# Performance work log

Measured on AMD Instinct MI355X. Metric: run time of the kernel, lower is better.

Reference implementation:

```python
import jax, jax.numpy as jnp
import numpy as np

EPS = 1e-7  # keras backend epsilon
ROUTINGS = 3

def squash(s, axis=-1):
    # v = ||s||^2/(1+||s||^2) * s/||s||
    sq = jnp.sum(jnp.square(s), axis=axis, keepdims=True)
    scale = sq / (1.0 + sq) / jnp.sqrt(sq + EPS)
    return scale * s

def setup_inputs() -> dict:
    key = jax.random.key(0)
    k1, k2 = jax.random.split(key)
    B, in_num, in_dim = 64, 2048, 16
    num_caps, dim_caps = 64, 32
    inputs = jax.random.normal(k1, (B, in_num, in_dim), dtype=jnp.float32)
    # glorot_uniform limit = sqrt(6/(fan_in+fan_out)) with fan_in=in_dim, fan_out=dim_caps
    limit = np.sqrt(6.0 / (in_dim + dim_caps)).astype(np.float32)
    W = jax.random.uniform(k2, (num_caps, in_num, dim_caps, in_dim),
                           dtype=jnp.float32, minval=-limit, maxval=limit)
    return {"inputs": inputs, "W": W}

def reference(inputs, W):
    # inputs: [b, i, l]; W: [j, i, k, l]
    # inputs_hat[b, j, i, k] = W[j, i, k, :] @ inputs[b, i, :]
    u_hat = jnp.einsum('jikl,bil->bjik', W, inputs)
    B, J, I, K = u_hat.shape
    b = jnp.zeros((B, J, I), dtype=u_hat.dtype)  # routing logits
    v = None
    for r in range(ROUTINGS):
        c = jax.nn.softmax(b, axis=1)                      # softmax over output capsules j
        s = jnp.einsum('bji,bjik->bjk', c, u_hat)          # weighted sum over input capsules
        v = squash(s)                                      # [b, j, k]
        if r < ROUTINGS - 1:
            b = b + jnp.einsum('bjk,bjik->bji', v, u_hat)  # agreement update
    return v  # [B, num_capsule, dim_capsule]
```

## Files before the change

kernel.cpp:

```cpp
#include <hip/hip_runtime.h>


#define B_ 64
#define I_ 2048
#define L_ 16
#define J_ 64
#define K_ 32
#define N_ 2048

typedef _Float16 half8_t __attribute__((ext_vector_type(8)));
typedef float f32x16 __attribute__((ext_vector_type(16)));
typedef float float4_t __attribute__((ext_vector_type(4)));

__device__ __forceinline__ f32x16 fzero16() {
    f32x16 z;
#pragma unroll
    for (int r = 0; r < 16; ++r) z[r] = 0.f;
    return z;
}

__global__ __launch_bounds__(256) void cast_x_kernel(const float* __restrict__ X,
                                                     _Float16* __restrict__ Xh) {
    unsigned tid = blockIdx.x * 256u + threadIdx.x;
    unsigned b = tid & 63u;
    unsigned i = tid >> 6;
    const float4_t* src = (const float4_t*)(X + (size_t)(b * I_ + i) * L_);
    float4_t f0 = src[0], f1 = src[1], f2 = src[2], f3 = src[3];
    half8_t h0, h1;
#pragma unroll
    for (int e = 0; e < 4; ++e) {
        h0[e] = (_Float16)f0[e];
        h0[4 + e] = (_Float16)f1[e];
        h1[e] = (_Float16)f2[e];
        h1[4 + e] = (_Float16)f3[e];
    }
    _Float16* dst = Xh + (size_t)(i * B_ + b) * L_;
    *(half8_t*)dst = h0;
    *(half8_t*)(dst + 8) = h1;
}

__global__ __launch_bounds__(512) void s0_cast_kernel(const float* __restrict__ Wf,
                                                      _Float16* __restrict__ Wh_out,
                                                      const _Float16* __restrict__ Xh,
                                                      _Float16* __restrict__ parts,
                                                      int SCH, int ICH) {
    const int tid = threadIdx.x;
    const int w = tid >> 6;
    const int l = tid & 63;
    const int h2 = l >> 5;
    const int kb = l & 31;
    const int chunk = blockIdx.x >> 3;
    const int jq = blockIdx.x & 7;
    const int j = jq * 8 + w;

    float s0[16], s1[16];
#pragma unroll
    for (int r = 0; r < 16; ++r) { s0[r] = 0.f; s1[r] = 0.f; }

    const int i0 = chunk * ICH;
    for (int ii = 0; ii < ICH; ++ii) {
        const int i = i0 + ii;
        const _Float16* xb = Xh + (size_t)i * (B_ * L_);
        half8_t xf0 = *(const half8_t*)(xb + kb * L_ + 8 * h2);
        half8_t xf1 = *(const half8_t*)(xb + (32 + kb) * L_ + 8 * h2);
        const float4_t* wsrc =
            (const float4_t*)(Wf + ((size_t)(j * I_ + i) * K_ + kb) * L_ + 8 * h2);
        float4_t a0 = wsrc[0], a1 = wsrc[1];
        half8_t af;
#pragma unroll
        for (int e = 0; e < 4; ++e) {
            af[e] = (_Float16)a0[e];
            af[4 + e] = (_Float16)a1[e];
        }
        *(half8_t*)(Wh_out + ((size_t)(i * J_ + j) * K_ + kb) * L_ + 8 * h2) = af;
        f32x16 acc0 = __builtin_amdgcn_mfma_f32_32x32x16_f16(af, xf0, fzero16(), 0, 0, 0);
        f32x16 acc1 = __builtin_amdgcn_mfma_f32_32x32x16_f16(af, xf1, fzero16(), 0, 0, 0);
#pragma unroll
        for (int r = 0; r < 16; ++r) {
            s0[r] += acc0[r];
            s1[r] += acc1[r];
        }
    }
#pragma unroll
    for (int r = 0; r < 16; ++r) {
        const int k = (r & 3) + 8 * (r >> 2) + 4 * h2;
        _Float16* p = parts + (((size_t)chunk * J_ + j) * K_ + k) * B_;
        p[kb] = (_Float16)s0[r];
        p[32 + kb] = (_Float16)s1[r];
    }
}

__global__ __launch_bounds__(512, 6) void zcalc_kernel(const _Float16* __restrict__ Wh,
                                                       const _Float16* __restrict__ Xh,
                                                       const _Float16* __restrict__ wvz,
                                                       _Float16* __restrict__ ebuf,
                                                       int SCH, int ICH) {
    const int tid = threadIdx.x;
    const int w = tid >> 6;
    const int l = tid & 63;
    const int h2 = l >> 5;
    const int kb = l & 31;
    const int chunk = blockIdx.x >> 3;
    const int jq = blockIdx.x & 7;
    const int j = jq * 8 + w;

    const _Float16* wp = wvz + ((size_t)(j * 2 + h2) * B_ + kb) * 16;
    const half8_t wv00 = *(const half8_t*)wp;
    const half8_t wv01 = *(const half8_t*)(wp + 8);
    const half8_t wv10 = *(const half8_t*)(wp + 512);
    const half8_t wv11 = *(const half8_t*)(wp + 520);

    const int i0 = chunk * ICH;
    for (int ii = 0; ii < ICH; ++ii) {
        const int i = i0 + ii;
        const _Float16* xb = Xh + (size_t)i * (B_ * L_);
        half8_t xf0 = *(const half8_t*)(xb + kb * L_ + 8 * h2);
        half8_t xf1 = *(const half8_t*)(xb + (32 + kb) * L_ + 8 * h2);
        half8_t af = *(const half8_t*)(Wh + ((size_t)(i * J_ + j) * K_ + kb) * L_ + 8 * h2);
        f32x16 acc0 = __builtin_amdgcn_mfma_f32_32x32x16_f16(af, xf0, fzero16(), 0, 0, 0);
        f32x16 acc1 = __builtin_amdgcn_mfma_f32_32x32x16_f16(af, xf1, fzero16(), 0, 0, 0);
        float z0a = 0.f, z0b = 0.f, z0c = 0.f, z0d = 0.f;
        float z1a = 0.f, z1b = 0.f, z1c = 0.f, z1d = 0.f;
#pragma unroll
        for (int r = 0; r < 4; ++r) {
            z0a += acc0[r]      * (float)wv00[r];
            z0b += acc0[r + 4]  * (float)wv00[r + 4];
            z0c += acc0[r + 8]  * (float)wv01[r];
            z0d += acc0[r + 12] * (float)wv01[r + 4];
            z1a += acc1[r]      * (float)wv10[r];
            z1b += acc1[r + 4]  * (float)wv10[r + 4];
            z1c += acc1[r + 8]  * (float)wv11[r];
            z1d += acc1[r + 12] * (float)wv11[r + 4];
        }
        float z0 = (z0a + z0b) + (z0c + z0d);
        float z1 = (z1a + z1b) + (z1c + z1d);
        z0 += __shfl_xor(z0, 32, 64);
        z1 += __shfl_xor(z1, 32, 64);
        const float zf = fminf((l < 32) ? z0 : z1, 11.0f);
        ebuf[((size_t)j * I_ + i) * B_ + l] = (_Float16)__expf(zf);
    }
}

__global__ __launch_bounds__(256, 8) void dsum_kernel(const _Float16* __restrict__ ebuf,
                                                      float* __restrict__ rD) {
    const int w = threadIdx.x >> 6;
    const int l = threadIdx.x & 63;
    const int i = blockIdx.x * 4 + w;
    float p0 = 0.f, p1 = 0.f, p2 = 0.f, p3 = 0.f;
#pragma unroll
    for (int jq = 0; jq < 16; ++jq) {
        p0 += (float)ebuf[((size_t)(jq * 4 + 0) * I_ + i) * B_ + l];
        p1 += (float)ebuf[((size_t)(jq * 4 + 1) * I_ + i) * B_ + l];
        p2 += (float)ebuf[((size_t)(jq * 4 + 2) * I_ + i) * B_ + l];
        p3 += (float)ebuf[((size_t)(jq * 4 + 3) * I_ + i) * B_ + l];
    }
    rD[i * B_ + l] = 1.0f / ((p0 + p1) + (p2 + p3));
}

__global__ __launch_bounds__(512) void s_kernel(const _Float16* __restrict__ Wh,
                                                const _Float16* __restrict__ Xh,
                                                const _Float16* __restrict__ ebuf,
                                                const float* __restrict__ rD,
                                                _Float16* __restrict__ parts,
                                                int SCH, int ICH) {
    const int tid = threadIdx.x;
    const int w = tid >> 6;
    const int l = tid & 63;
    const int h2 = l >> 5;
    const int kb = l & 31;
    const int chunk = blockIdx.x >> 3;
    const int jq = blockIdx.x & 7;
    const int j = jq * 8 + w;

    float s0[16], s1[16];
#pragma unroll
    for (int r = 0; r < 16; ++r) { s0[r] = 0.f; s1[r] = 0.f; }

    const int i0 = chunk * ICH;
    for (int ii = 0; ii < ICH; ++ii) {
        const int i = i0 + ii;
        const _Float16* xb = Xh + (size_t)i * (B_ * L_);
        half8_t xf0 = *(const half8_t*)(xb + kb * L_ + 8 * h2);
        half8_t xf1 = *(const half8_t*)(xb + (32 + kb) * L_ + 8 * h2);
        half8_t af = *(const half8_t*)(Wh + ((size_t)(i * J_ + j) * K_ + kb) * L_ + 8 * h2);
        const _Float16* ep = ebuf + ((size_t)j * I_ + i) * B_;
        const float c0 = (float)ep[kb] * rD[i * B_ + kb];
        const float c1 = (float)ep[32 + kb] * rD[i * B_ + 32 + kb];
        f32x16 acc0 = __builtin_amdgcn_mfma_f32_32x32x16_f16(af, xf0, fzero16(), 0, 0, 0);
        f32x16 acc1 = __builtin_amdgcn_mfma_f32_32x32x16_f16(af, xf1, fzero16(), 0, 0, 0);
#pragma unroll
        for (int r = 0; r < 16; ++r) {
            s0[r] += c0 * acc0[r];
            s1[r] += c1 * acc1[r];
        }
    }
#pragma unroll
    for (int r = 0; r < 16; ++r) {
        const int k = (r & 3) + 8 * (r >> 2) + 4 * h2;
        _Float16* p = parts + (((size_t)chunk * J_ + j) * K_ + k) * B_;
        p[kb] = (_Float16)s0[r];
        p[32 + kb] = (_Float16)s1[r];
    }
}

__global__ __launch_bounds__(512) void reduce_kernel(const _Float16* __restrict__ parts,
                                                     _Float16* __restrict__ wvz,
                                                     float* __restrict__ out,
                                                     int SCH, int STEP) {
    __shared__ float ssql[8][64];
    const int j = blockIdx.x;
    const int t = threadIdx.x;
    const int b = t & 63;
    const int kg = t >> 6;

    float acc[4] = {0.f, 0.f, 0.f, 0.f};
    for (int ch = 0; ch < SCH; ++ch) {
        const _Float16* p = parts + (((size_t)ch * J_ + j) * K_ + kg * 4) * B_ + b;
#pragma unroll
        for (int q = 0; q < 4; ++q) acc[q] += (float)p[(size_t)q * B_];
    }
    if (STEP == 0) {
#pragma unroll
        for (int q = 0; q < 4; ++q) acc[q] *= (1.0f / 64.0f);
    }
    ssql[kg][b] = acc[0] * acc[0] + acc[1] * acc[1] + acc[2] * acc[2] + acc[3] * acc[3];
    __syncthreads();
    float sq = 0.f;
#pragma unroll
    for (int g = 0; g < 8; ++g) sq += ssql[g][b];
    const float scale = sq / (1.0f + sq) / sqrtf(sq + 1e-7f);

    if (STEP == 2) {
#pragma unroll
        for (int q = 0; q < 4; ++q)
            out[(size_t)b * N_ + j * K_ + kg * 4 + q] = acc[q] * scale;
    } else {
        _Float16* wp = wvz + ((size_t)(j * 2 + (kg & 1)) * B_ + b) * 16 + 4 * (kg >> 1);
#pragma unroll
        for (int q = 0; q < 4; ++q) {
            const float prev = (STEP == 0) ? 0.f : (float)wp[q];
            wp[q] = (_Float16)(prev + acc[q] * scale);
        }
    }
}

extern "C" void kernel_launch(void* const* d_in, const int* in_sizes, int n_in,
                              void* d_out, int out_size, void* d_ws, size_t ws_size,
                              hipStream_t stream) {
    const float* X = (const float*)d_in[0];
    const float* W = (const float*)d_in[1];
    float* out = (float*)d_out;
    char* ws = (char*)d_ws;

    const size_t WH_BYTES = (size_t)I_ * J_ * K_ * L_ * 2;
    const size_t XH_BYTES = (size_t)I_ * B_ * L_ * 2;
    const size_t WVZ_BYTES = (size_t)J_ * 2 * B_ * 16 * 2;
    const size_t EB_BYTES = (size_t)J_ * I_ * B_ * 2;
    const size_t RD_BYTES = (size_t)I_ * B_ * 4;
    const size_t FIX = WH_BYTES + XH_BYTES + WVZ_BYTES + EB_BYTES + RD_BYTES;

    int SCH = 64;
    if (ws_size < FIX + (size_t)64 * N_ * B_ * 2) SCH = 32;
    if (ws_size < FIX + (size_t)32 * N_ * B_ * 2) SCH = 16;
    const int ICH = I_ / SCH;

    _Float16* Wh = (_Float16*)ws;
    _Float16* Xh = (_Float16*)(ws + WH_BYTES);
    _Float16* wvz = (_Float16*)(ws + WH_BYTES + XH_BYTES);
    _Float16* ebuf = (_Float16*)(ws + WH_BYTES + XH_BYTES + WVZ_BYTES);
    float* rD = (float*)(ws + WH_BYTES + XH_BYTES + WVZ_BYTES + EB_BYTES);
    _Float16* parts = (_Float16*)(ws + FIX);

    cast_x_kernel<<<dim3((B_ * I_) / 256), dim3(256), 0, stream>>>(X, Xh);

    s0_cast_kernel<<<dim3(SCH * 8), dim3(512), 0, stream>>>(W, Wh, Xh, parts, SCH, ICH);
    reduce_kernel<<<dim3(J_), dim3(512), 0, stream>>>(parts, wvz, out, SCH, 0);

    zcalc_kernel<<<dim3(SCH * 8), dim3(512), 0, stream>>>(Wh, Xh, wvz, ebuf, SCH, ICH);
    dsum_kernel<<<dim3(I_ / 4), dim3(256), 0, stream>>>(ebuf, rD);
    s_kernel<<<dim3(SCH * 8), dim3(512), 0, stream>>>(Wh, Xh, ebuf, rD, parts, SCH, ICH);
    reduce_kernel<<<dim3(J_), dim3(512), 0, stream>>>(parts, wvz, out, SCH, 1);

    zcalc_kernel<<<dim3(SCH * 8), dim3(512), 0, stream>>>(Wh, Xh, wvz, ebuf, SCH, ICH);
    dsum_kernel<<<dim3(I_ / 4), dim3(256), 0, stream>>>(ebuf, rD);
    s_kernel<<<dim3(SCH * 8), dim3(512), 0, stream>>>(Wh, Xh, ebuf, rD, parts, SCH, ICH);
    reduce_kernel<<<dim3(J_), dim3(512), 0, stream>>>(parts, wvz, out, SCH, 2);

    (void)in_sizes; (void)n_in; (void)out_size;
}
```

Before: 305.9 us.

## Fuse softmax denominator sum into zcalc via shared-memory reduce and atomics

```diff
diff --git a/kernel.cpp b/kernel.cpp
--- a/kernel.cpp
+++ b/kernel.cpp
@@ -90,11 +90,13 @@
     }
 }
 
-__global__ __launch_bounds__(512, 6) void zcalc_kernel(const _Float16* __restrict__ Wh,
-                                                       const _Float16* __restrict__ Xh,
-                                                       const _Float16* __restrict__ wvz,
-                                                       _Float16* __restrict__ ebuf,
-                                                       int SCH, int ICH) {
+__global__ __launch_bounds__(512) void zcalc_kernel(const _Float16* __restrict__ Wh,
+                                                    const _Float16* __restrict__ Xh,
+                                                    const _Float16* __restrict__ wvz,
+                                                    _Float16* __restrict__ ebuf,
+                                                    float* __restrict__ D,
+                                                    int SCH, int ICH) {
+    __shared__ float es[8][8][64];
     const int tid = threadIdx.x;
     const int w = tid >> 6;
     const int l = tid & 63;
@@ -111,56 +113,54 @@
     const half8_t wv11 = *(const half8_t*)(wp + 520);
 
     const int i0 = chunk * ICH;
-    for (int ii = 0; ii < ICH; ++ii) {
-        const int i = i0 + ii;
-        const _Float16* xb = Xh + (size_t)i * (B_ * L_);
-        half8_t xf0 = *(const half8_t*)(xb + kb * L_ + 8 * h2);
-        half8_t xf1 = *(const half8_t*)(xb + (32 + kb) * L_ + 8 * h2);
-        half8_t af = *(const half8_t*)(Wh + ((size_t)(i * J_ + j) * K_ + kb) * L_ + 8 * h2);
-        f32x16 acc0 = __builtin_amdgcn_mfma_f32_32x32x16_f16(af, xf0, fzero16(), 0, 0, 0);
-        f32x16 acc1 = __builtin_amdgcn_mfma_f32_32x32x16_f16(af, xf1, fzero16(), 0, 0, 0);
-        float z0a = 0.f, z0b = 0.f, z0c = 0.f, z0d = 0.f;
-        float z1a = 0.f, z1b = 0.f, z1c = 0.f, z1d = 0.f;
-#pragma unroll
-        for (int r = 0; r < 4; ++r) {
-            z0a += acc0[r]      * (float)wv00[r];
-            z0b += acc0[r + 4]  * (float)wv00[r + 4];
-            z0c += acc0[r + 8]  * (float)wv01[r];
-            z0d += acc0[r + 12] * (float)wv01[r + 4];
-            z1a += acc1[r]      * (float)wv10[r];
-            z1b += acc1[r + 4]  * (float)wv10[r + 4];
-            z1c += acc1[r + 8]  * (float)wv11[r];
-            z1d += acc1[r + 12] * (float)wv11[r + 4];
-        }
-        float z0 = (z0a + z0b) + (z0c + z0d);
-        float z1 = (z1a + z1b) + (z1c + z1d);
-        z0 += __shfl_xor(z0, 32, 64);
-        z1 += __shfl_xor(z1, 32, 64);
-        const float zf = fminf((l < 32) ? z0 : z1, 11.0f);
-        ebuf[((size_t)j * I_ + i) * B_ + l] = (_Float16)__expf(zf);
-    }
-}
-
-__global__ __launch_bounds__(256, 8) void dsum_kernel(const _Float16* __restrict__ ebuf,
-                                                      float* __restrict__ rD) {
-    const int w = threadIdx.x >> 6;
-    const int l = threadIdx.x & 63;
-    const int i = blockIdx.x * 4 + w;
-    float p0 = 0.f, p1 = 0.f, p2 = 0.f, p3 = 0.f;
-#pragma unroll
-    for (int jq = 0; jq < 16; ++jq) {
-        p0 += (float)ebuf[((size_t)(jq * 4 + 0) * I_ + i) * B_ + l];
-        p1 += (float)ebuf[((size_t)(jq * 4 + 1) * I_ + i) * B_ + l];
-        p2 += (float)ebuf[((size_t)(jq * 4 + 2) * I_ + i) * B_ + l];
-        p3 += (float)ebuf[((size_t)(jq * 4 + 3) * I_ + i) * B_ + l];
-    }
-    rD[i * B_ + l] = 1.0f / ((p0 + p1) + (p2 + p3));
+    for (int it = 0; it < ICH; it += 8) {
+#pragma unroll
+        for (int q = 0; q < 8; ++q) {
+            const int i = i0 + it + q;
+            const _Float16* xb = Xh + (size_t)i * (B_ * L_);
+            half8_t xf0 = *(const half8_t*)(xb + kb * L_ + 8 * h2);
+            half8_t xf1 = *(const half8_t*)(xb + (32 + kb) * L_ + 8 * h2);
+            half8_t af = *(const half8_t*)(Wh + ((size_t)(i * J_ + j) * K_ + kb) * L_ + 8 * h2);
+            f32x16 acc0 = __builtin_amdgcn_mfma_f32_32x32x16_f16(af, xf0, fzero16(), 0, 0, 0);
+            f32x16 acc1 = __builtin_amdgcn_mfma_f32_32x32x16_f16(af, xf1, fzero16(), 0, 0, 0);
+            float z0a = 0.f, z0b = 0.f, z0c = 0.f, z0d = 0.f;
+            float z1a = 0.f, z1b = 0.f, z1c = 0.f, z1d = 0.f;
+#pragma unroll
+            for (int r = 0; r < 4; ++r) {
+                z0a += acc0[r]      * (float)wv00[r];
+                z0b += acc0[r + 4]  * (float)wv00[r + 4];
+                z0c += acc0[r + 8]  * (float)wv01[r];
+                z0d += acc0[r + 12] * (float)wv01[r + 4];
+                z1a += acc1[r]      * (float)wv10[r];
+                z1b += acc1[r + 4]  * (float)wv10[r + 4];
+                z1c += acc1[r + 8]  * (float)wv11[r];
+                z1d += acc1[r + 12] * (float)wv11[r + 4];
+            }
+            float z0 = (z0a + z0b) + (z0c + z0d);
+            float z1 = (z1a + z1b) + (z1c + z1d);
+            z0 += __shfl_xor(z0, 32, 64);
+            z1 += __shfl_xor(z1, 32, 64);
+            const float zf = fminf((l < 32) ? z0 : z1, 11.0f);
+            const float ev = __expf(zf);
+            ebuf[((size_t)j * I_ + i) * B_ + l] = (_Float16)ev;
+            es[w][q][l] = ev;
+        }
+        __syncthreads();
+        {
+            float p0 = es[0][w][l] + es[1][w][l];
+            float p1 = es[2][w][l] + es[3][w][l];
+            float p2 = es[4][w][l] + es[5][w][l];
+            float p3 = es[6][w][l] + es[7][w][l];
+            atomicAdd(&D[(size_t)(i0 + it + w) * B_ + l], (p0 + p1) + (p2 + p3));
+        }
+        __syncthreads();
+    }
 }
 
 __global__ __launch_bounds__(512) void s_kernel(const _Float16* __restrict__ Wh,
                                                 const _Float16* __restrict__ Xh,
                                                 const _Float16* __restrict__ ebuf,
-                                                const float* __restrict__ rD,
+                                                const float* __restrict__ D,
                                                 _Float16* __restrict__ parts,
                                                 int SCH, int ICH) {
     const int tid = threadIdx.x;
@@ -184,8 +184,8 @@
         half8_t xf1 = *(const half8_t*)(xb + (32 + kb) * L_ + 8 * h2);
         half8_t af = *(const half8_t*)(Wh + ((size_t)(i * J_ + j) * K_ + kb) * L_ + 8 * h2);
         const _Float16* ep = ebuf + ((size_t)j * I_ + i) * B_;
-        const float c0 = (float)ep[kb] * rD[i * B_ + kb];
-        const float c1 = (float)ep[32 + kb] * rD[i * B_ + 32 + kb];
+        const float c0 = (float)ep[kb] * __builtin_amdgcn_rcpf(D[(size_t)i * B_ + kb]);
+        const float c1 = (float)ep[32 + kb] * __builtin_amdgcn_rcpf(D[(size_t)i * B_ + 32 + kb]);
         f32x16 acc0 = __builtin_amdgcn_mfma_f32_32x32x16_f16(af, xf0, fzero16(), 0, 0, 0);
         f32x16 acc1 = __builtin_amdgcn_mfma_f32_32x32x16_f16(af, xf1, fzero16(), 0, 0, 0);
 #pragma unroll
@@ -206,12 +206,18 @@
 __global__ __launch_bounds__(512) void reduce_kernel(const _Float16* __restrict__ parts,
                                                      _Float16* __restrict__ wvz,
                                                      float* __restrict__ out,
+                                                     float* __restrict__ D,
                                                      int SCH, int STEP) {
     __shared__ float ssql[8][64];
     const int j = blockIdx.x;
     const int t = threadIdx.x;
     const int b = t & 63;
     const int kg = t >> 6;
+
+    if (STEP < 2) {
+        float4_t zz = {0.f, 0.f, 0.f, 0.f};
+        ((float4_t*)D)[(size_t)j * 512 + t] = zz;
+    }
 
     float acc[4] = {0.f, 0.f, 0.f, 0.f};
     for (int ch = 0; ch < SCH; ++ch) {
@@ -256,8 +262,8 @@
     const size_t XH_BYTES = (size_t)I_ * B_ * L_ * 2;
     const size_t WVZ_BYTES = (size_t)J_ * 2 * B_ * 16 * 2;
     const size_t EB_BYTES = (size_t)J_ * I_ * B_ * 2;
-    const size_t RD_BYTES = (size_t)I_ * B_ * 4;
-    const size_t FIX = WH_BYTES + XH_BYTES + WVZ_BYTES + EB_BYTES + RD_BYTES;
+    const size_t D_BYTES = (size_t)I_ * B_ * 4;
+    const size_t FIX = WH_BYTES + XH_BYTES + WVZ_BYTES + EB_BYTES + D_BYTES;
 
     int SCH = 64;
     if (ws_size < FIX + (size_t)64 * N_ * B_ * 2) SCH = 32;
@@ -268,23 +274,21 @@
     _Float16* Xh = (_Float16*)(ws + WH_BYTES);
     _Float16* wvz = (_Float16*)(ws + WH_BYTES + XH_BYTES);
     _Float16* ebuf = (_Float16*)(ws + WH_BYTES + XH_BYTES + WVZ_BYTES);
-    float* rD = (float*)(ws + WH_BYTES + XH_BYTES + WVZ_BYTES + EB_BYTES);
+    float* D = (float*)(ws + WH_BYTES + XH_BYTES + WVZ_BYTES + EB_BYTES);
     _Float16* parts = (_Float16*)(ws + FIX);
 
     cast_x_kernel<<<dim3((B_ * I_) / 256), dim3(256), 0, stream>>>(X, Xh);
 
     s0_cast_kernel<<<dim3(SCH * 8), dim3(512), 0, stream>>>(W, Wh, Xh, parts, SCH, ICH);
-    reduce_kernel<<<dim3(J_), dim3(512), 0, stream>>>(parts, wvz, out, SCH, 0);
-
-    zcalc_kernel<<<dim3(SCH * 8), dim3(512), 0, stream>>>(Wh, Xh, wvz, ebuf, SCH, ICH);
-    dsum_kernel<<<dim3(I_ / 4), dim3(256), 0, stream>>>(ebuf, rD);
-    s_kernel<<<dim3(SCH * 8), dim3(512), 0, stream>>>(Wh, Xh, ebuf, rD, parts, SCH, ICH);
-    reduce_kernel<<<dim3(J_), dim3(512), 0, stream>>>(parts, wvz, out, SCH, 1);
-
-    zcalc_kernel<<<dim3(SCH * 8), dim3(512), 0, stream>>>(Wh, Xh, wvz, ebuf, SCH, ICH);
-    dsum_kernel<<<dim3(I_ / 4), dim3(256), 0, stream>>>(ebuf, rD);
-    s_kernel<<<dim3(SCH * 8), dim3(512), 0, stream>>>(Wh, Xh, ebuf, rD, parts, SCH, ICH);
-    reduce_kernel<<<dim3(J_), dim3(512), 0, stream>>>(parts, wvz, out, SCH, 2);
+    reduce_kernel<<<dim3(J_), dim3(512), 0, stream>>>(parts, wvz, out, D, SCH, 0);
+
+    zcalc_kernel<<<dim3(SCH * 8), dim3(512), 0, stream>>>(Wh, Xh, wvz, ebuf, D, SCH, ICH);
+    s_kernel<<<dim3(SCH * 8), dim3(512), 0, stream>>>(Wh, Xh, ebuf, D, parts, SCH, ICH);
+    reduce_kernel<<<dim3(J_), dim3(512), 0, stream>>>(parts, wvz, out, D, SCH, 1);
+
+    zcalc_kernel<<<dim3(SCH * 8), dim3(512), 0, stream>>>(Wh, Xh, wvz, ebuf, D, SCH, ICH);
+    s_kernel<<<dim3(SCH * 8), dim3(512), 0, stream>>>(Wh, Xh, ebuf, D, parts, SCH, ICH);
+    reduce_kernel<<<dim3(J_), dim3(512), 0, stream>>>(parts, wvz, out, D, SCH, 2);
 
     (void)in_sizes; (void)n_in; (void)out_size;
 }
```

New measurement: 292.4 us. 1.05x faster.
